# Kernel optimization log

Measured on AMD Instinct MI355X. Metric: run time of the kernel, lower is better.

## Reference

```python
import jax, jax.numpy as jnp
import numpy as np

IN_DIM = 512
OUT_DIM = 512

def setup_inputs() -> dict:
    key = jax.random.key(0)
    k1, k2, k3, k4 = jax.random.split(key, 4)
    B, N, D = 8, 2048, IN_DIM
    Q = jax.random.normal(k1, (B, N, D), dtype=jnp.float32)
    K = jax.random.normal(k2, (B, N, D), dtype=jnp.float32)
    V = jax.random.normal(k3, (B, N, D), dtype=jnp.float32)
    # nn.Linear(in_dim, out_dim, bias=False): weight shape [out_dim, in_dim]
    W = jax.random.normal(k4, (OUT_DIM, IN_DIM), dtype=jnp.float32) / np.sqrt(IN_DIM)
    scale_param = jnp.ones((1,), dtype=jnp.float32)
    a = jnp.ones((1,), dtype=jnp.float32)
    b = jnp.ones((1,), dtype=jnp.float32)
    return {"Q": Q, "K": K, "V": V, "W": W, "scale_param": scale_param, "a": a, "b": b}

def reference(Q, K, V, W, scale_param, a, b):
    inv_sqrt_d = 1.0 / np.sqrt(OUT_DIM).astype(np.float32)
    # [B,N,N] attention scores
    scores = jnp.einsum('bnd,bmd->bnm', Q, K) * scale_param * inv_sqrt_d
    attn = jax.nn.softmax(scores, axis=-1)
    R = jax.nn.relu(jnp.einsum('bnm,bmd->bnd', attn, V))
    C = jax.nn.relu(jnp.einsum('bnd,od->bno', V - R, W))
    return a * R + b * C
```

## Files before the change

### kernel.cpp

```cpp
#include <hip/hip_runtime.h>

typedef __attribute__((ext_vector_type(8))) short bf16x8;
typedef __attribute__((ext_vector_type(4))) float f32x4;
typedef unsigned int u32;
typedef unsigned short u16;

__device__ __forceinline__ u16 f2bf(float f) {
  u32 u = __float_as_uint(f);
  u += 0x7fffu + ((u >> 16) & 1u);
  return (u16)(u >> 16);
}
__device__ __forceinline__ u32 pack2(float a, float b) {
  return (u32)f2bf(a) | ((u32)f2bf(b) << 16);
}
__device__ __forceinline__ void gload_lds16(const void* g, void* l) {
  __builtin_amdgcn_global_load_lds(
      (const __attribute__((address_space(1))) u32*)g,
      (__attribute__((address_space(3))) u32*)l, 16, 0, 0);
}

__global__ void cvt_bf16_kernel(const float* __restrict__ in, u16* __restrict__ out,
                                long long n8) {
  long long i = (long long)blockIdx.x * blockDim.x + threadIdx.x;
  if (i >= n8) return;
  const float4* p = (const float4*)in + i * 2;
  float4 a = p[0], b = p[1];
  uint4 o;
  o.x = pack2(a.x, a.y); o.y = pack2(a.z, a.w);
  o.z = pack2(b.x, b.y); o.w = pack2(b.z, b.w);
  ((uint4*)out)[i] = o;
}

__global__ __launch_bounds__(256)
void transpose_v_kernel(const float* __restrict__ V, u16* __restrict__ Vt) {
  __shared__ float tile[64][65];
  const int n0 = blockIdx.x * 64, d0 = blockIdx.y * 64, bat = blockIdx.z;
  const int t = threadIdx.x;
  const int rr = t >> 4, cc = (t & 15) * 4;
#pragma unroll
  for (int i = 0; i < 4; ++i) {
    int r = i * 16 + rr;
    float4 v = *(const float4*)(V + ((size_t)(bat * 2048 + n0 + r)) * 512 + d0 + cc);
    tile[r][cc + 0] = v.x; tile[r][cc + 1] = v.y;
    tile[r][cc + 2] = v.z; tile[r][cc + 3] = v.w;
  }
  __syncthreads();
#pragma unroll
  for (int i = 0; i < 4; ++i) {
    int dr = i * 16 + rr;
    uint2 o;
    o.x = pack2(tile[cc + 0][dr], tile[cc + 1][dr]);
    o.y = pack2(tile[cc + 2][dr], tile[cc + 3][dr]);
    *(uint2*)(Vt + ((size_t)(bat * 512 + d0 + dr)) * 2048 + n0 + cc) = o;
  }
}

#define ATT_LDS 80672

__global__ __launch_bounds__(512, 2)
void attn_kernel(const float* __restrict__ Qf, const u16* __restrict__ Kb,
                 const u16* __restrict__ Vtg, const float* __restrict__ Vg,
                 const u16* __restrict__ Wb, const float* __restrict__ sp,
                 const float* __restrict__ ap, const float* __restrict__ bp,
                 float* __restrict__ Out) {
  extern __shared__ char smem[];
  u16* Ks0 = (u16*)smem;
  u16* Ks1 = (u16*)(smem + 32768);
  float* Ss = (float*)(smem + 65536);
  u16* Ps = (u16*)(smem + 74752);
  float* mrow = (float*)(smem + 79872);
  float* lrow = (float*)(smem + 80128);
  float* resc = (float*)(smem + 80384);
  u32* flg = (u32*)(smem + 80640);

  const int tid = threadIdx.x, lane = tid & 63, wid = tid >> 6;
  const int bat = blockIdx.x, q0 = blockIdx.y * 64;
  const float scale = sp[0] * 0.04419417382415922f;
  const int l15 = lane & 15, l4 = lane >> 4;
  const int srow = tid >> 3, sseg = tid & 7;
  const int rwD = wid >> 1, cwD = wid & 1;

  {
    const float* qsrc = Qf + ((size_t)(bat * 2048 + q0 + srow)) * 512;
    char* qdst = smem + srow * 1024;
    const int sw = (srow & 7) << 4;
#pragma unroll
    for (int j = 0; j < 8; ++j) {
      int sc = sseg * 8 + j;
      float4 x0 = *(const float4*)(qsrc + sc * 8);
      float4 x1 = *(const float4*)(qsrc + sc * 8 + 4);
      uint4 w;
      w.x = pack2(x0.x * scale, x0.y * scale); w.y = pack2(x0.z * scale, x0.w * scale);
      w.z = pack2(x1.x * scale, x1.y * scale); w.w = pack2(x1.z * scale, x1.w * scale);
      *(uint4*)(qdst + ((sc * 16) ^ sw)) = w;
    }
  }
  __syncthreads();

  bf16x8 qf[16];
  {
    const char* qb = smem + (rwD * 16 + l15) * 1024;
    const int swA = (l15 & 7) << 4;
#pragma unroll
    for (int ks = 0; ks < 16; ++ks)
      qf[ks] = *(const bf16x8*)(qb + ((ks * 64 + l4 * 16) ^ swA));
  }
  __syncthreads();

#pragma unroll
  for (int j = 0; j < 4; ++j) {
    int row = wid * 4 + j;
    gload_lds16(Kb + ((size_t)(bat * 2048 + row)) * 512 + ((lane ^ (row & 7)) * 8),
                (char*)Ks0 + row * 1024);
  }
  if (tid < 64) { mrow[tid] = -1e30f; lrow[tid] = 0.f; }

  f32x4 o[4][4];
#pragma unroll
  for (int a = 0; a < 4; ++a)
#pragma unroll
    for (int b = 0; b < 4; ++b) o[a][b] = (f32x4){0.f, 0.f, 0.f, 0.f};

  __syncthreads();

  const int swB = (l15 & 7) << 4;

  for (int it = 0; it < 64; ++it) {
    const u16* Kcur = (it & 1) ? Ks1 : Ks0;
    u16* Knxt = (it & 1) ? Ks0 : Ks1;

    uint4 vreg[4];
#pragma unroll
    for (int cf = 0; cf < 4; ++cf)
      vreg[cf] = *(const uint4*)(Vtg +
          ((size_t)(bat * 512 + wid * 64 + cf * 16 + l15)) * 2048 +
          it * 32 + l4 * 8);

    if (it < 63) {
      const int kv1 = (it + 1) * 32;
#pragma unroll
      for (int j = 0; j < 4; ++j) {
        int row = wid * 4 + j;
        gload_lds16(Kb + ((size_t)(bat * 2048 + kv1 + row)) * 512 + ((lane ^ (row & 7)) * 8),
                    (char*)Knxt + row * 1024);
      }
    }
    __builtin_amdgcn_sched_barrier(0);

    {
      f32x4 se = (f32x4){0.f, 0.f, 0.f, 0.f};
      f32x4 so = (f32x4){0.f, 0.f, 0.f, 0.f};
      const char* kb = (const char*)Kcur + (cwD * 16 + l15) * 1024;
      __builtin_amdgcn_s_setprio(1);
#pragma unroll
      for (int ks = 0; ks < 16; ks += 2) {
        const int offe = (ks * 64 + l4 * 16) ^ swB;
        const int offo = ((ks + 1) * 64 + l4 * 16) ^ swB;
        bf16x8 be = *(const bf16x8*)(kb + offe);
        bf16x8 bo = *(const bf16x8*)(kb + offo);
        se = __builtin_amdgcn_mfma_f32_16x16x32_bf16(qf[ks], be, se, 0, 0, 0);
        so = __builtin_amdgcn_mfma_f32_16x16x32_bf16(qf[ks + 1], bo, so, 0, 0, 0);
      }
      __builtin_amdgcn_s_setprio(0);
      f32x4 s = se + so;
      const int r0 = rwD * 16 + l4 * 4;
      const int c0 = cwD * 16 + l15;
#pragma unroll
      for (int j = 0; j < 4; ++j) Ss[(r0 + j) * 36 + c0] = s[j];
    }
    __syncthreads();

    {
      const int row = srow, g = sseg;
      float4 sv = *(const float4*)(Ss + row * 36 + g * 4);
      float mt = fmaxf(fmaxf(sv.x, sv.y), fmaxf(sv.z, sv.w));
#pragma unroll
      for (int off = 1; off < 8; off <<= 1) mt = fmaxf(mt, __shfl_xor(mt, off));
      const float mold = mrow[row];
      const bool exceed = (mt > mold + 8.0f);
      const float mnew = exceed ? mt : mold;
      float p0 = __expf(sv.x - mnew), p1 = __expf(sv.y - mnew);
      float p2 = __expf(sv.z - mnew), p3 = __expf(sv.w - mnew);
      float ps = (p0 + p1) + (p2 + p3);
#pragma unroll
      for (int off = 1; off < 8; off <<= 1) ps += __shfl_xor(ps, off);
      if (g == 0) {
        float rs = exceed ? __expf(mold - mnew) : 1.0f;
        resc[row] = rs;
        lrow[row] = lrow[row] * rs + ps;
        mrow[row] = mnew;
      }
      int ex = __any(g == 0 && exceed);
      if (lane == 0) flg[wid] = ex ? 1u : 0u;
      uint2 pw;
      pw.x = pack2(p0, p1); pw.y = pack2(p2, p3);
      *(uint2*)((char*)Ps + row * 80 + g * 8) = pw;
    }
    __syncthreads();

    {
      const uint4* fp = (const uint4*)flg;
      uint4 fa = fp[0], fb = fp[1];
      u32 anyr = fa.x | fa.y | fa.z | fa.w | fb.x | fb.y | fb.z | fb.w;
      if (anyr) {
#pragma unroll
        for (int fr = 0; fr < 4; ++fr) {
          f32x4 rf = *(const f32x4*)(resc + fr * 16 + l4 * 4);
#pragma unroll
          for (int cf = 0; cf < 4; ++cf)
#pragma unroll
            for (int j = 0; j < 4; ++j) o[fr][cf][j] *= rf[j];
        }
      }
      bf16x8 pa[4];
#pragma unroll
      for (int fr = 0; fr < 4; ++fr)
        pa[fr] = *(const bf16x8*)((const char*)Ps + (fr * 16 + l15) * 80 + l4 * 16);
      __builtin_amdgcn_s_setprio(1);
#pragma unroll
      for (int fr = 0; fr < 4; ++fr)
#pragma unroll
        for (int cf = 0; cf < 4; ++cf)
          o[fr][cf] = __builtin_amdgcn_mfma_f32_16x16x32_bf16(
              pa[fr], *(const bf16x8*)&vreg[cf], o[fr][cf], 0, 0, 0);
      __builtin_amdgcn_s_setprio(0);
    }
  }

  const float av = ap[0], bv = bp[0];
#pragma unroll
  for (int fr = 0; fr < 4; ++fr) {
    f32x4 lv = *(const f32x4*)(lrow + fr * 16 + l4 * 4);
    f32x4 inv;
#pragma unroll
    for (int j = 0; j < 4; ++j) inv[j] = 1.f / lv[j];
#pragma unroll
    for (int cf = 0; cf < 4; ++cf)
#pragma unroll
      for (int j = 0; j < 4; ++j)
        o[fr][cf][j] = fmaxf(o[fr][cf][j] * inv[j], 0.f);
  }
  {
    u16* Ts = (u16*)smem;
#pragma unroll
    for (int fr = 0; fr < 4; ++fr)
#pragma unroll
      for (int cf = 0; cf < 4; ++cf) {
        const int col = wid * 64 + cf * 16 + l15;
#pragma unroll
        for (int j = 0; j < 4; ++j) {
          const int row = fr * 16 + l4 * 4 + j;
          float v = Vg[((size_t)(bat * 2048 + q0 + row)) * 512 + col];
          u16 t = f2bf(v - o[fr][cf][j]);
          *(u16*)((char*)Ts + row * 1024 + ((col * 2) ^ ((row & 7) << 4))) = t;
        }
      }
  }
  __syncthreads();

  f32x4 c2[4][4];
#pragma unroll
  for (int a = 0; a < 4; ++a)
#pragma unroll
    for (int b = 0; b < 4; ++b) c2[a][b] = (f32x4){0.f, 0.f, 0.f, 0.f};
  {
    const u16* Ts = (u16*)smem;
#pragma unroll
    for (int ks = 0; ks < 16; ++ks) {
      bf16x8 aT[4];
#pragma unroll
      for (int fr = 0; fr < 4; ++fr) {
        const int row = fr * 16 + l15;
        aT[fr] = *(const bf16x8*)((const char*)Ts + row * 1024 +
                                  ((ks * 64 + l4 * 16) ^ ((row & 7) << 4)));
      }
#pragma unroll
      for (int cf = 0; cf < 4; ++cf) {
        const int orow = wid * 64 + cf * 16 + l15;
        bf16x8 bw = *(const bf16x8*)(Wb + (size_t)orow * 512 + ks * 32 + l4 * 8);
#pragma unroll
        for (int fr = 0; fr < 4; ++fr)
          c2[fr][cf] = __builtin_amdgcn_mfma_f32_16x16x32_bf16(aT[fr], bw, c2[fr][cf], 0, 0, 0);
      }
    }
  }
#pragma unroll
  for (int fr = 0; fr < 4; ++fr)
#pragma unroll
    for (int cf = 0; cf < 4; ++cf) {
      const int col = wid * 64 + cf * 16 + l15;
#pragma unroll
      for (int j = 0; j < 4; ++j) {
        const int row = fr * 16 + l4 * 4 + j;
        float c = fmaxf(c2[fr][cf][j], 0.f);
        Out[((size_t)(bat * 2048 + q0 + row)) * 512 + col] = av * o[fr][cf][j] + bv * c;
      }
    }
}

extern "C" void kernel_launch(void* const* d_in, const int* in_sizes, int n_in,
                              void* d_out, int out_size, void* d_ws, size_t ws_size,
                              hipStream_t stream) {
  const float* Q = (const float*)d_in[0];
  const float* K = (const float*)d_in[1];
  const float* V = (const float*)d_in[2];
  const float* W = (const float*)d_in[3];
  const float* sp = (const float*)d_in[4];
  const float* ap = (const float*)d_in[5];
  const float* bp = (const float*)d_in[6];
  float* out = (float*)d_out;

  const long long tEl = 8LL * 2048 * 512;
  u16* Kb = (u16*)d_ws;
  u16* Vt = Kb + tEl;
  u16* Wb = Vt + tEl;

  cvt_bf16_kernel<<<4096, 256, 0, stream>>>(K, Kb, tEl / 8);
  cvt_bf16_kernel<<<128, 256, 0, stream>>>(W, Wb, (512LL * 512) / 8);
  transpose_v_kernel<<<dim3(32, 8, 8), 256, 0, stream>>>(V, Vt);

  hipFuncSetAttribute(reinterpret_cast<const void*>(attn_kernel),
                      hipFuncAttributeMaxDynamicSharedMemorySize, ATT_LDS);
  attn_kernel<<<dim3(8, 32), 512, ATT_LDS, stream>>>(Q, Kb, Vt, V, Wb, sp, ap, bp, out);
}
```

Baseline: 183.0 us.

## Halve query tile to 32 rows, widen KV tile to 64, single-buffer K

Reworks the attention tiling so each block handles 32 query rows instead of 64 while each iteration consumes 64 keys instead of 32, doubling the grid to 512 blocks. K double buffering is dropped in favour of one buffer refilled after the score barrier, and Q is loaded straight into registers without staging through LDS. Launch bounds move to 4 blocks per CU to raise occupancy and fill more CUs. The trade-offs are lost K prefetch overlap, K and W reloaded by twice as many blocks, and V loads that now sit on the critical path after the softmax barrier. LDS use is about 79 KB per block, so four resident blocks would not fit in the 160 KB LDS listed for MI355X.

```diff
diff --git a/kernel.cpp b/kernel.cpp
--- a/kernel.cpp
+++ b/kernel.cpp
@@ -55,102 +55,67 @@
   }
 }
 
-#define ATT_LDS 80672
-
-__global__ __launch_bounds__(512, 2)
+#define ATT_LDS 79264
+
+__global__ __launch_bounds__(512, 4)
 void attn_kernel(const float* __restrict__ Qf, const u16* __restrict__ Kb,
                  const u16* __restrict__ Vtg, const float* __restrict__ Vg,
                  const u16* __restrict__ Wb, const float* __restrict__ sp,
                  const float* __restrict__ ap, const float* __restrict__ bp,
                  float* __restrict__ Out) {
   extern __shared__ char smem[];
-  u16* Ks0 = (u16*)smem;
-  u16* Ks1 = (u16*)(smem + 32768);
+  u16* Ks = (u16*)smem;
   float* Ss = (float*)(smem + 65536);
-  u16* Ps = (u16*)(smem + 74752);
-  float* mrow = (float*)(smem + 79872);
-  float* lrow = (float*)(smem + 80128);
-  float* resc = (float*)(smem + 80384);
-  u32* flg = (u32*)(smem + 80640);
+  u16* Ps = (u16*)(smem + 74240);
+  float* mrow = (float*)(smem + 78848);
+  float* lrow = (float*)(smem + 78976);
+  float* resc = (float*)(smem + 79104);
+  u32* flg = (u32*)(smem + 79232);
 
   const int tid = threadIdx.x, lane = tid & 63, wid = tid >> 6;
-  const int bat = blockIdx.x, q0 = blockIdx.y * 64;
+  const int bat = blockIdx.x, q0 = blockIdx.y * 32;
   const float scale = sp[0] * 0.04419417382415922f;
   const int l15 = lane & 15, l4 = lane >> 4;
-  const int srow = tid >> 3, sseg = tid & 7;
-  const int rwD = wid >> 1, cwD = wid & 1;
-
+  const int srow = tid >> 4, sseg = tid & 15;
+  const int rwD = wid >> 2, cwD = wid & 3;
+
+  bf16x8 qf[16];
   {
-    const float* qsrc = Qf + ((size_t)(bat * 2048 + q0 + srow)) * 512;
-    char* qdst = smem + srow * 1024;
-    const int sw = (srow & 7) << 4;
-#pragma unroll
-    for (int j = 0; j < 8; ++j) {
-      int sc = sseg * 8 + j;
-      float4 x0 = *(const float4*)(qsrc + sc * 8);
-      float4 x1 = *(const float4*)(qsrc + sc * 8 + 4);
+    const float* qsrc = Qf + ((size_t)(bat * 2048 + q0 + rwD * 16 + l15)) * 512;
+#pragma unroll
+    for (int ks = 0; ks < 16; ++ks) {
+      float4 x0 = *(const float4*)(qsrc + ks * 32 + l4 * 8);
+      float4 x1 = *(const float4*)(qsrc + ks * 32 + l4 * 8 + 4);
       uint4 w;
       w.x = pack2(x0.x * scale, x0.y * scale); w.y = pack2(x0.z * scale, x0.w * scale);
       w.z = pack2(x1.x * scale, x1.y * scale); w.w = pack2(x1.z * scale, x1.w * scale);
-      *(uint4*)(qdst + ((sc * 16) ^ sw)) = w;
-    }
-  }
+      qf[ks] = *(bf16x8*)&w;
+    }
+  }
+
+#pragma unroll
+  for (int j = 0; j < 8; ++j) {
+    int row = wid * 8 + j;
+    gload_lds16(Kb + ((size_t)(bat * 2048 + row)) * 512 + ((lane ^ (row & 7)) * 8),
+                (char*)Ks + row * 1024);
+  }
+  if (tid < 32) { mrow[tid] = -1e30f; lrow[tid] = 0.f; }
+
+  f32x4 o[2][4];
+#pragma unroll
+  for (int a = 0; a < 2; ++a)
+#pragma unroll
+    for (int b = 0; b < 4; ++b) o[a][b] = (f32x4){0.f, 0.f, 0.f, 0.f};
+
   __syncthreads();
 
-  bf16x8 qf[16];
-  {
-    const char* qb = smem + (rwD * 16 + l15) * 1024;
-    const int swA = (l15 & 7) << 4;
-#pragma unroll
-    for (int ks = 0; ks < 16; ++ks)
-      qf[ks] = *(const bf16x8*)(qb + ((ks * 64 + l4 * 16) ^ swA));
-  }
-  __syncthreads();
-
-#pragma unroll
-  for (int j = 0; j < 4; ++j) {
-    int row = wid * 4 + j;
-    gload_lds16(Kb + ((size_t)(bat * 2048 + row)) * 512 + ((lane ^ (row & 7)) * 8),
-                (char*)Ks0 + row * 1024);
-  }
-  if (tid < 64) { mrow[tid] = -1e30f; lrow[tid] = 0.f; }
-
-  f32x4 o[4][4];
-#pragma unroll
-  for (int a = 0; a < 4; ++a)
-#pragma unroll
-    for (int b = 0; b < 4; ++b) o[a][b] = (f32x4){0.f, 0.f, 0.f, 0.f};
-
-  __syncthreads();
-
   const int swB = (l15 & 7) << 4;
 
-  for (int it = 0; it < 64; ++it) {
-    const u16* Kcur = (it & 1) ? Ks1 : Ks0;
-    u16* Knxt = (it & 1) ? Ks0 : Ks1;
-
-    uint4 vreg[4];
-#pragma unroll
-    for (int cf = 0; cf < 4; ++cf)
-      vreg[cf] = *(const uint4*)(Vtg +
-          ((size_t)(bat * 512 + wid * 64 + cf * 16 + l15)) * 2048 +
-          it * 32 + l4 * 8);
-
-    if (it < 63) {
-      const int kv1 = (it + 1) * 32;
-#pragma unroll
-      for (int j = 0; j < 4; ++j) {
-        int row = wid * 4 + j;
-        gload_lds16(Kb + ((size_t)(bat * 2048 + kv1 + row)) * 512 + ((lane ^ (row & 7)) * 8),
-                    (char*)Knxt + row * 1024);
-      }
-    }
-    __builtin_amdgcn_sched_barrier(0);
-
+  for (int it = 0; it < 32; ++it) {
     {
       f32x4 se = (f32x4){0.f, 0.f, 0.f, 0.f};
       f32x4 so = (f32x4){0.f, 0.f, 0.f, 0.f};
-      const char* kb = (const char*)Kcur + (cwD * 16 + l15) * 1024;
+      const char* kb = (const char*)Ks + (cwD * 16 + l15) * 1024;
       __builtin_amdgcn_s_setprio(1);
 #pragma unroll
       for (int ks = 0; ks < 16; ks += 2) {
@@ -166,16 +131,26 @@
       const int r0 = rwD * 16 + l4 * 4;
       const int c0 = cwD * 16 + l15;
 #pragma unroll
-      for (int j = 0; j < 4; ++j) Ss[(r0 + j) * 36 + c0] = s[j];
+      for (int j = 0; j < 4; ++j) Ss[(r0 + j) * 68 + c0] = s[j];
     }
     __syncthreads();
+
+    if (it < 31) {
+      const int kv1 = (it + 1) * 64;
+#pragma unroll
+      for (int j = 0; j < 8; ++j) {
+        int row = wid * 8 + j;
+        gload_lds16(Kb + ((size_t)(bat * 2048 + kv1 + row)) * 512 + ((lane ^ (row & 7)) * 8),
+                    (char*)Ks + row * 1024);
+      }
+    }
 
     {
       const int row = srow, g = sseg;
-      float4 sv = *(const float4*)(Ss + row * 36 + g * 4);
+      float4 sv = *(const float4*)(Ss + row * 68 + g * 4);
       float mt = fmaxf(fmaxf(sv.x, sv.y), fmaxf(sv.z, sv.w));
 #pragma unroll
-      for (int off = 1; off < 8; off <<= 1) mt = fmaxf(mt, __shfl_xor(mt, off));
+      for (int off = 1; off < 16; off <<= 1) mt = fmaxf(mt, __shfl_xor(mt, off));
       const float mold = mrow[row];
       const bool exceed = (mt > mold + 8.0f);
       const float mnew = exceed ? mt : mold;
@@ -183,7 +158,7 @@
       float p2 = __expf(sv.z - mnew), p3 = __expf(sv.w - mnew);
       float ps = (p0 + p1) + (p2 + p3);
 #pragma unroll
-      for (int off = 1; off < 8; off <<= 1) ps += __shfl_xor(ps, off);
+      for (int off = 1; off < 16; off <<= 1) ps += __shfl_xor(ps, off);
       if (g == 0) {
         float rs = exceed ? __expf(mold - mnew) : 1.0f;
         resc[row] = rs;
@@ -194,17 +169,25 @@
       if (lane == 0) flg[wid] = ex ? 1u : 0u;
       uint2 pw;
       pw.x = pack2(p0, p1); pw.y = pack2(p2, p3);
-      *(uint2*)((char*)Ps + row * 80 + g * 8) = pw;
+      *(uint2*)((char*)Ps + row * 144 + g * 8) = pw;
     }
     __syncthreads();
 
     {
+      uint4 vr[8];
+#pragma unroll
+      for (int s = 0; s < 2; ++s)
+#pragma unroll
+        for (int cf = 0; cf < 4; ++cf)
+          vr[s * 4 + cf] = *(const uint4*)(Vtg +
+              ((size_t)(bat * 512 + wid * 64 + cf * 16 + l15)) * 2048 +
+              it * 64 + s * 32 + l4 * 8);
       const uint4* fp = (const uint4*)flg;
       uint4 fa = fp[0], fb = fp[1];
       u32 anyr = fa.x | fa.y | fa.z | fa.w | fb.x | fb.y | fb.z | fb.w;
       if (anyr) {
 #pragma unroll
-        for (int fr = 0; fr < 4; ++fr) {
+        for (int fr = 0; fr < 2; ++fr) {
           f32x4 rf = *(const f32x4*)(resc + fr * 16 + l4 * 4);
 #pragma unroll
           for (int cf = 0; cf < 4; ++cf)
@@ -212,24 +195,27 @@
             for (int j = 0; j < 4; ++j) o[fr][cf][j] *= rf[j];
         }
       }
-      bf16x8 pa[4];
-#pragma unroll
-      for (int fr = 0; fr < 4; ++fr)
-        pa[fr] = *(const bf16x8*)((const char*)Ps + (fr * 16 + l15) * 80 + l4 * 16);
-      __builtin_amdgcn_s_setprio(1);
-#pragma unroll
-      for (int fr = 0; fr < 4; ++fr)
-#pragma unroll
-        for (int cf = 0; cf < 4; ++cf)
-          o[fr][cf] = __builtin_amdgcn_mfma_f32_16x16x32_bf16(
-              pa[fr], *(const bf16x8*)&vreg[cf], o[fr][cf], 0, 0, 0);
-      __builtin_amdgcn_s_setprio(0);
+#pragma unroll
+      for (int s = 0; s < 2; ++s) {
+        bf16x8 pa[2];
+#pragma unroll
+        for (int fr = 0; fr < 2; ++fr)
+          pa[fr] = *(const bf16x8*)((const char*)Ps + (fr * 16 + l15) * 144 + s * 64 + l4 * 16);
+        __builtin_amdgcn_s_setprio(1);
+#pragma unroll
+        for (int fr = 0; fr < 2; ++fr)
+#pragma unroll
+          for (int cf = 0; cf < 4; ++cf)
+            o[fr][cf] = __builtin_amdgcn_mfma_f32_16x16x32_bf16(
+                pa[fr], *(const bf16x8*)&vr[s * 4 + cf], o[fr][cf], 0, 0, 0);
+        __builtin_amdgcn_s_setprio(0);
+      }
     }
   }
 
   const float av = ap[0], bv = bp[0];
 #pragma unroll
-  for (int fr = 0; fr < 4; ++fr) {
+  for (int fr = 0; fr < 2; ++fr) {
     f32x4 lv = *(const f32x4*)(lrow + fr * 16 + l4 * 4);
     f32x4 inv;
 #pragma unroll
@@ -243,7 +229,7 @@
   {
     u16* Ts = (u16*)smem;
 #pragma unroll
-    for (int fr = 0; fr < 4; ++fr)
+    for (int fr = 0; fr < 2; ++fr)
 #pragma unroll
       for (int cf = 0; cf < 4; ++cf) {
         const int col = wid * 64 + cf * 16 + l15;
@@ -258,18 +244,18 @@
   }
   __syncthreads();
 
-  f32x4 c2[4][4];
-#pragma unroll
-  for (int a = 0; a < 4; ++a)
+  f32x4 c2[2][4];
+#pragma unroll
+  for (int a = 0; a < 2; ++a)
 #pragma unroll
     for (int b = 0; b < 4; ++b) c2[a][b] = (f32x4){0.f, 0.f, 0.f, 0.f};
   {
     const u16* Ts = (u16*)smem;
 #pragma unroll
     for (int ks = 0; ks < 16; ++ks) {
-      bf16x8 aT[4];
-#pragma unroll
-      for (int fr = 0; fr < 4; ++fr) {
+      bf16x8 aT[2];
+#pragma unroll
+      for (int fr = 0; fr < 2; ++fr) {
         const int row = fr * 16 + l15;
         aT[fr] = *(const bf16x8*)((const char*)Ts + row * 1024 +
                                   ((ks * 64 + l4 * 16) ^ ((row & 7) << 4)));
@@ -279,13 +265,13 @@
         const int orow = wid * 64 + cf * 16 + l15;
         bf16x8 bw = *(const bf16x8*)(Wb + (size_t)orow * 512 + ks * 32 + l4 * 8);
 #pragma unroll
-        for (int fr = 0; fr < 4; ++fr)
+        for (int fr = 0; fr < 2; ++fr)
           c2[fr][cf] = __builtin_amdgcn_mfma_f32_16x16x32_bf16(aT[fr], bw, c2[fr][cf], 0, 0, 0);
       }
     }
   }
 #pragma unroll
-  for (int fr = 0; fr < 4; ++fr)
+  for (int fr = 0; fr < 2; ++fr)
 #pragma unroll
     for (int cf = 0; cf < 4; ++cf) {
       const int col = wid * 64 + cf * 16 + l15;
@@ -321,5 +307,5 @@
 
   hipFuncSetAttribute(reinterpret_cast<const void*>(attn_kernel),
                       hipFuncAttributeMaxDynamicSharedMemorySize, ATT_LDS);
-  attn_kernel<<<dim3(8, 32), 512, ATT_LDS, stream>>>(Q, Kb, Vt, V, Wb, sp, ap, bp, out);
-}
+  attn_kernel<<<dim3(8, 64), 512, ATT_LDS, stream>>>(Q, Kb, Vt, V, Wb, sp, ap, bp, out);
+}
```

New measurement: 662.8 us. 262% more time.
